# Optimization experiments

Hardware: AMD Instinct MI355X
Metric: run time of the kernel (lower is better)

## Reference

```python
import jax, jax.numpy as jnp
import numpy as np

N_NODES = 50000
IN_FT = 64
OUT_FT = 64
J = 3
MAX_SCALE = 2 ** (J - 1)  # 4
TOTAL_DIM = IN_FT * (1 + (J - 1) + J * (J - 1) // 2)  # 6*IN_FT = 384
N_EDGES = 800000


def setup_inputs() -> dict:
    key = jax.random.key(0)
    k1, k2, k3, k4, k5 = jax.random.split(key, 5)
    seq = jax.random.normal(k1, (N_NODES, IN_FT), dtype=jnp.float32)
    edge_index = jax.random.randint(k2, (2, N_EDGES), 0, N_NODES, dtype=jnp.int32)
    edge_weight = jax.random.uniform(k3, (N_EDGES,), dtype=jnp.float32)
    # xavier_normal_ with gain=1.414 on fc.weight [OUT_FT, TOTAL_DIM]
    std = 1.414 * np.sqrt(2.0 / (OUT_FT + TOTAL_DIM))
    fc_w = jax.random.normal(k4, (OUT_FT, TOTAL_DIM), dtype=jnp.float32) * std
    bias = jnp.zeros((OUT_FT,), dtype=jnp.float32)
    prelu_a = jnp.array(0.25, dtype=jnp.float32)  # nn.PReLU default single param
    return {"seq": seq, "edge_index": edge_index, "edge_weight": edge_weight,
            "fc_w": fc_w, "bias": bias, "prelu_a": prelu_a}


def reference(seq, edge_index, edge_weight, fc_w, bias, prelu_a):
    n = seq.shape[0]
    f = seq.shape[1]
    src, dst = edge_index[0], edge_index[1]

    def spmm(x):  # gather source features, scale by edge weight, scatter-add to dest
        return jax.ops.segment_sum(x[src] * edge_weight[:, None], dst, num_segments=n)

    diff_list = []
    x_curr = seq
    for step in range(1, MAX_SCALE + 1):
        x_curr = spmm(x_curr)
        if step & (step - 1) == 0:
            diff_list.append(x_curr)

    F0 = diff_list[-1]
    F1 = jnp.concatenate([jnp.abs(diff_list[i - 1] - diff_list[i])
                          for i in range(1, len(diff_list))], axis=1)

    # second-order features: diffuse concatenated U, take abs diffs of blocks
    U = jnp.concatenate(diff_list, axis=1)  # [N, J*f]
    U_diff = [U]
    for _ in range(1, MAX_SCALE):
        U_diff.append(spmm(U_diff[-1]))
    feats2 = []
    for j in range(J):
        for jp in range(j + 1, J):
            s, e = j * f, (j + 1) * f
            feats2.append(jnp.abs(U_diff[jp][:, s:e] - U_diff[jp - 1][:, s:e]))
    F2 = jnp.concatenate(feats2, axis=1)

    feats = jnp.concatenate([F0, F1, F2], axis=1)  # [N, 6*f]
    out = feats @ fc_w.T + bias
    return jnp.where(out > 0, out, prelu_a * out)
```

## Files before the change

kernel.cpp:

```cpp
#include <hip/hip_runtime.h>
#include <hip/hip_bf16.h>

typedef short short8 __attribute__((ext_vector_type(8)));
typedef float f32x4 __attribute__((ext_vector_type(4)));

static constexpr int F = 64;
static constexpr int TOT = 384;
static constexpr int SLOT = 64;
static constexpr int CAP = 1536;
static constexpr int EPB = 4096;
static constexpr int WPN = 20480;

__device__ __forceinline__ unsigned short f2bf(float f) {
    unsigned u = __builtin_bit_cast(unsigned, f);
    u += 0x7fffu + ((u >> 16) & 1u);
    return (unsigned short)(u >> 16);
}
__device__ __forceinline__ float bflo(unsigned u) {
    return __builtin_bit_cast(float, u << 16);
}
__device__ __forceinline__ float bfhi(unsigned u) {
    return __builtin_bit_cast(float, u & 0xffff0000u);
}


__global__ __launch_bounds__(256) void combo_kernel(
    const float* __restrict__ x, unsigned* __restrict__ xb,
    const float* __restrict__ fcw, unsigned short* __restrict__ wp,
    int* __restrict__ gcur, long long total8, int cvtblocks, int nbuck)
{
    int b = blockIdx.x;
    if (b < cvtblocks) {
        long long i = (long long)b * 256 + threadIdx.x;
        if (i >= total8) return;
        const float4 f0 = *(const float4*)(x + i * 8);
        const float4 f1 = *(const float4*)(x + i * 8 + 4);
        uint4 o;
        o.x = (unsigned)f2bf(f0.x) | ((unsigned)f2bf(f0.y) << 16);
        o.y = (unsigned)f2bf(f0.z) | ((unsigned)f2bf(f0.w) << 16);
        o.z = (unsigned)f2bf(f1.x) | ((unsigned)f2bf(f1.y) << 16);
        o.w = (unsigned)f2bf(f1.z) | ((unsigned)f2bf(f1.w) << 16);
        *(uint4*)(xb + i * 4) = o;
    } else if (b == cvtblocks) {
        for (int e = threadIdx.x; e < WPN; e += 256) {
            int j = e & 7;
            int l = (e >> 3) & 63;
            int t = (e >> 9) & 3;
            int s = e >> 11;
            int k  = s * 32 + ((l >> 4) << 3) + j;
            int nn = t * 16 + (l & 15);
            int c  = k & 63;
            float v;
            if (k < 64)       v = fcw[nn * TOT + c];
            else if (k < 128) v = fcw[nn * TOT + 64 + c] + fcw[nn * TOT + 192 + c];
            else if (k < 192) v = fcw[nn * TOT + 128 + c];
            else if (k < 256) v = fcw[nn * TOT + 256 + c];
            else              v = fcw[nn * TOT + 320 + c];
            wp[e] = f2bf(v);
        }
    } else {
        for (int i = threadIdx.x; i < nbuck; i += 256) gcur[i] = 0;
    }
}


__global__ __launch_bounds__(256) void scatter_bucket(
    const int* __restrict__ src, const int* __restrict__ dst,
    const float* __restrict__ ew, int* __restrict__ gcur,
    int2* __restrict__ ebuf, int ne)
{
    __shared__ int hist[1024];
    __shared__ int base[1024];
    for (int i = threadIdx.x; i < 1024; i += 256) hist[i] = 0;
    __syncthreads();

    long long b0 = (long long)blockIdx.x * EPB;
    int sv[16]; int dv[16]; float wv[16];
#pragma unroll
    for (int j = 0; j < 4; ++j) {
        long long i = b0 + (long long)(threadIdx.x + 256 * j) * 4;
        if (i + 3 < ne) {
            int4   s = *(const int4*)(src + i);
            int4   d = *(const int4*)(dst + i);
            float4 w = *(const float4*)(ew + i);
            sv[j*4+0]=s.x; sv[j*4+1]=s.y; sv[j*4+2]=s.z; sv[j*4+3]=s.w;
            dv[j*4+0]=d.x; dv[j*4+1]=d.y; dv[j*4+2]=d.z; dv[j*4+3]=d.w;
            wv[j*4+0]=w.x; wv[j*4+1]=w.y; wv[j*4+2]=w.z; wv[j*4+3]=w.w;
        } else {
#pragma unroll
            for (int c = 0; c < 4; ++c) {
                long long e = i + c;
                if (e < ne) { sv[j*4+c]=src[e]; dv[j*4+c]=dst[e]; wv[j*4+c]=ew[e]; }
                else dv[j*4+c] = -1;
            }
        }
    }
#pragma unroll
    for (int c = 0; c < 16; ++c)
        if (dv[c] >= 0) atomicAdd(&hist[dv[c] >> 6], 1);
    __syncthreads();
    for (int i = threadIdx.x; i < 1024; i += 256) {
        int h = hist[i];
        base[i] = h ? atomicAdd(&gcur[i], h) : 0;
        hist[i] = 0;
    }
    __syncthreads();
#pragma unroll
    for (int c = 0; c < 16; ++c) {
        int d = dv[c];
        if (d < 0) continue;
        int b = d >> 6;
        int p = base[b] + atomicAdd(&hist[b], 1);
        if (p < CAP)
            ebuf[(long long)b * CAP + p] =
                make_int2(sv[c] | ((d & 63) << 26), __float_as_int(wv[c]));
    }
}


__global__ __launch_bounds__(256) void bucket_to_slots(
    const int2* __restrict__ ebuf, const int* __restrict__ gcur,
    unsigned* __restrict__ csr4, int* __restrict__ cnt, int n)
{
    __shared__ int lcnt[64];
    int b = blockIdx.x;
    if (threadIdx.x < 64) lcnt[threadIdx.x] = 0;
    __syncthreads();
    int m = min(gcur[b], CAP);
    long long eb = (long long)b * CAP;
    for (int i = threadIdx.x; i < m; i += 256) {
        int2 r = ebuf[eb + i];
        int dl = (r.x >> 26) & 63;
        int s  = r.x & 0x03ffffff;
        int p  = atomicAdd(&lcnt[dl], 1);
        if (p < SLOT) {
            long long node = ((long long)b << 6) + dl;
            csr4[(node << 6) + p] =
                (unsigned)s | ((unsigned)f2bf(__int_as_float(r.y)) << 16);
        }
    }
    __syncthreads();
    if (threadIdx.x < 64) {
        int node = (b << 6) + threadIdx.x;
        if (node < n) cnt[node] = min(lcnt[threadIdx.x], SLOT);
    }
}


__global__ __launch_bounds__(256) void spmm_bf16(
    const unsigned short* __restrict__ xb, unsigned short* __restrict__ yb,
    const int* __restrict__ cnt, const unsigned* __restrict__ csr4, int n)
{
    int wid  = (blockIdx.x * 256 + threadIdx.x) >> 6;
    int lane = threadIdx.x & 63;
    if (wid >= n) return;
    int deg = min(cnt[wid], SLOT);
    long long beg = (long long)wid << 6;
    int g  = lane >> 3;
    int fi = lane & 7;

    float a0[8], a1[8];
#pragma unroll
    for (int i = 0; i < 8; ++i) { a0[i] = 0.f; a1[i] = 0.f; }

    for (int k = 0; k < deg; k += 16) {
        int e0 = k + 2 * g;
        unsigned r0 = 0u, r1 = 0u;
        if (e0 < deg) {
            uint2 rr = *(const uint2*)(csr4 + beg + e0);
            r0 = rr.x;
            if (e0 + 1 < deg) r1 = rr.y;
        }
        int   s0 = (int)(r0 & 0xffffu), s1 = (int)(r1 & 0xffffu);
        float w0 = bfhi(r0),            w1 = bfhi(r1);
        uint4 xa = *(const uint4*)(xb + (long long)s0 * F + fi * 8);
        uint4 xc = *(const uint4*)(xb + (long long)s1 * F + fi * 8);
        a0[0] += w0 * bflo(xa.x); a0[1] += w0 * bfhi(xa.x);
        a0[2] += w0 * bflo(xa.y); a0[3] += w0 * bfhi(xa.y);
        a0[4] += w0 * bflo(xa.z); a0[5] += w0 * bfhi(xa.z);
        a0[6] += w0 * bflo(xa.w); a0[7] += w0 * bfhi(xa.w);
        a1[0] += w1 * bflo(xc.x); a1[1] += w1 * bfhi(xc.x);
        a1[2] += w1 * bflo(xc.y); a1[3] += w1 * bfhi(xc.y);
        a1[4] += w1 * bflo(xc.z); a1[5] += w1 * bfhi(xc.z);
        a1[6] += w1 * bflo(xc.w); a1[7] += w1 * bfhi(xc.w);
    }
#pragma unroll
    for (int i = 0; i < 8; ++i) a0[i] += a1[i];
#pragma unroll
    for (int m = 8; m < 64; m <<= 1) {
#pragma unroll
        for (int i = 0; i < 8; ++i) a0[i] += __shfl_xor(a0[i], m, 64);
    }
    if (lane < 8) {
        uint4 o;
        o.x = (unsigned)f2bf(a0[0]) | ((unsigned)f2bf(a0[1]) << 16);
        o.y = (unsigned)f2bf(a0[2]) | ((unsigned)f2bf(a0[3]) << 16);
        o.z = (unsigned)f2bf(a0[4]) | ((unsigned)f2bf(a0[5]) << 16);
        o.w = (unsigned)f2bf(a0[6]) | ((unsigned)f2bf(a0[7]) << 16);
        *(uint4*)(yb + (long long)wid * F + fi * 8) = o;
    }
}


__global__ __launch_bounds__(256) void gemm_mfma2(
    const unsigned short* __restrict__ y1, const unsigned short* __restrict__ y2,
    const unsigned short* __restrict__ y3, const unsigned short* __restrict__ y4,
    const unsigned short* __restrict__ wp, const float* __restrict__ bias,
    const float* __restrict__ pa, float* __restrict__ out, int n)
{
    int lane = threadIdx.x & 63;
    int wid  = (blockIdx.x * 256 + threadIdx.x) >> 6;
    int m0   = wid * 16;
    if (m0 >= n) return;

    int r  = m0 + (lane & 15);
    int cb = (lane >> 4) * 8;
    float yv0[16], yv1[16], yv2[16], yv3[16];
    {
        const unsigned short* b0 = y1 + (long long)r * F;
        const unsigned short* b1 = y2 + (long long)r * F;
        const unsigned short* b2 = y3 + (long long)r * F;
        const unsigned short* b3 = y4 + (long long)r * F;
#define LOADSEG(dstv, bp)                                                     \
        {                                                                     \
            uint4 u0 = *(const uint4*)((bp) + cb);                            \
            uint4 u1 = *(const uint4*)((bp) + 32 + cb);                       \
            dstv[0]  = bflo(u0.x); dstv[1]  = bfhi(u0.x);                     \
            dstv[2]  = bflo(u0.y); dstv[3]  = bfhi(u0.y);                     \
            dstv[4]  = bflo(u0.z); dstv[5]  = bfhi(u0.z);                     \
            dstv[6]  = bflo(u0.w); dstv[7]  = bfhi(u0.w);                     \
            dstv[8]  = bflo(u1.x); dstv[9]  = bfhi(u1.x);                     \
            dstv[10] = bflo(u1.y); dstv[11] = bfhi(u1.y);                     \
            dstv[12] = bflo(u1.z); dstv[13] = bfhi(u1.z);                     \
            dstv[14] = bflo(u1.w); dstv[15] = bfhi(u1.w);                     \
        }
        LOADSEG(yv0, b0)
        LOADSEG(yv1, b1)
        LOADSEG(yv2, b2)
        LOADSEG(yv3, b3)
#undef LOADSEG
    }

    const short8* wps = (const short8*)wp;

    f32x4 acc0 = {0.f, 0.f, 0.f, 0.f};
    f32x4 acc1 = acc0, acc2 = acc0, acc3 = acc0;

#pragma unroll
    for (int s = 0; s < 10; ++s) {
        const int fb = s >> 1;
        const int h  = s & 1;
        short8 af;
#pragma unroll
        for (int j = 0; j < 8; ++j) {
            int ci = h * 8 + j;
            float fv;
            if (fb == 0)      fv = yv3[ci];
            else if (fb == 1) fv = fabsf(yv0[ci] - yv1[ci]);
            else if (fb == 2) fv = fabsf(yv1[ci] - yv3[ci]);
            else if (fb == 3) fv = fabsf(yv2[ci] - yv1[ci]);
            else              fv = fabsf(yv3[ci] - yv2[ci]);
            af[j] = (short)f2bf(fv);
        }
        short8 bf0 = wps[(s * 4 + 0) * 64 + lane];
        short8 bf1 = wps[(s * 4 + 1) * 64 + lane];
        short8 bf2 = wps[(s * 4 + 2) * 64 + lane];
        short8 bf3 = wps[(s * 4 + 3) * 64 + lane];
        acc0 = __builtin_amdgcn_mfma_f32_16x16x32_bf16(af, bf0, acc0, 0, 0, 0);
        acc1 = __builtin_amdgcn_mfma_f32_16x16x32_bf16(af, bf1, acc1, 0, 0, 0);
        acc2 = __builtin_amdgcn_mfma_f32_16x16x32_bf16(af, bf2, acc2, 0, 0, 0);
        acc3 = __builtin_amdgcn_mfma_f32_16x16x32_bf16(af, bf3, acc3, 0, 0, 0);
    }

    float a = pa[0];
    int orow = m0 + (lane >> 4) * 4;
    int ocol = lane & 15;
#define WRITE_T(accv, t)                                                      \
    {                                                                         \
        float bco = bias[(t) * 16 + ocol];                                    \
        _Pragma("unroll")                                                     \
        for (int v = 0; v < 4; ++v) {                                         \
            float val = accv[v] + bco;                                        \
            val = val > 0.f ? val : a * val;                                  \
            out[(long long)(orow + v) * F + (t) * 16 + ocol] = val;           \
        }                                                                     \
    }
    WRITE_T(acc0, 0)
    WRITE_T(acc1, 1)
    WRITE_T(acc2, 2)
    WRITE_T(acc3, 3)
#undef WRITE_T
}

extern "C" void kernel_launch(void* const* d_in, const int* in_sizes, int n_in,
                              void* d_out, int out_size, void* d_ws, size_t ws_size,
                              hipStream_t stream)
{
    const float* seq  = (const float*)d_in[0];
    const int*   eidx = (const int*)d_in[1];
    const float* ew   = (const float*)d_in[2];
    const float* fcw  = (const float*)d_in[3];
    const float* bias = (const float*)d_in[4];
    const float* pa   = (const float*)d_in[5];
    float* out = (float*)d_out;

    int n  = in_sizes[0] / F;
    int ne = in_sizes[2];
    const int* src = eidx;
    const int* dst = eidx + ne;

    long long nF = (long long)n * F;
    int nbuck = (n + 63) >> 6;

    unsigned short* xb  = (unsigned short*)d_ws;
    unsigned short* yb1 = xb  + nF;
    unsigned short* yb2 = yb1 + nF;
    unsigned short* yb3 = yb2 + nF;
    unsigned short* yb4 = yb3 + nF;
    int2* ebuf = (int2*)yb3;
    unsigned* csr4 = (unsigned*)(yb4 + nF);
    int*  cnt  = (int*)(csr4 + (long long)n * SLOT);
    int*  gcur = cnt + ((n + 3) & ~3);
    unsigned short* wp = (unsigned short*)(gcur + ((nbuck + 3) & ~3));

    long long total8 = nF / 8;
    int cvtblocks = (int)((total8 + 255) / 256);
    combo_kernel<<<cvtblocks + 2, 256, 0, stream>>>(
        seq, (unsigned*)xb, fcw, wp, gcur, total8, cvtblocks, nbuck);

    int bb = (ne + EPB - 1) / EPB;
    scatter_bucket<<<bb, 256, 0, stream>>>(src, dst, ew, gcur, ebuf, ne);
    bucket_to_slots<<<nbuck, 256, 0, stream>>>(ebuf, gcur, csr4, cnt, n);

    int sb = (int)((nF + 255) / 256);
    spmm_bf16<<<sb, 256, 0, stream>>>(xb,  yb1, cnt, csr4, n);
    spmm_bf16<<<sb, 256, 0, stream>>>(yb1, yb2, cnt, csr4, n);
    spmm_bf16<<<sb, 256, 0, stream>>>(yb2, yb3, cnt, csr4, n);
    spmm_bf16<<<sb, 256, 0, stream>>>(yb3, yb4, cnt, csr4, n);

    int gw = (n + 15) / 16;
    int gb = (gw * 64 + 255) / 256;
    gemm_mfma2<<<gb, 256, 0, stream>>>(yb1, yb2, yb3, yb4, wp, bias, pa, out, n);
}
```

Measured before the change: 140.4 us.

## Sort nodes by degree and process eight nodes per wave in SpMM

Builds a degree histogram, a prefix scan and a counting sort, so that nodes with equal degree are grouped into the same wavefront. Each wave then handles 8 nodes with 8 lanes per node, which removes the cross-lane shuffle reduction, and each lane walks its node's edges four at a time with vector loads. The goal is less divergence and less wasted lane work for the low average degree (~16). In exchange it adds two small kernels, one of them a single-threaded scan, global atomics and an indirection through the order array, and it loses the contiguous node locality of the output writes.

```diff
diff --git a/kernel.cpp b/kernel.cpp
--- a/kernel.cpp
+++ b/kernel.cpp
@@ -27,7 +27,8 @@
 __global__ __launch_bounds__(256) void combo_kernel(
     const float* __restrict__ x, unsigned* __restrict__ xb,
     const float* __restrict__ fcw, unsigned short* __restrict__ wp,
-    int* __restrict__ gcur, long long total8, int cvtblocks, int nbuck)
+    int* __restrict__ gcur, int* __restrict__ dhist, int* __restrict__ dcur,
+    long long total8, int cvtblocks, int nbuck)
 {
     int b = blockIdx.x;
     if (b < cvtblocks) {
@@ -60,6 +61,7 @@
         }
     } else {
         for (int i = threadIdx.x; i < nbuck; i += 256) gcur[i] = 0;
+        if (threadIdx.x < 65) { dhist[threadIdx.x] = 0; dcur[threadIdx.x] = 0; }
     }
 }
 
@@ -120,7 +122,8 @@
 
 __global__ __launch_bounds__(256) void bucket_to_slots(
     const int2* __restrict__ ebuf, const int* __restrict__ gcur,
-    unsigned* __restrict__ csr4, int* __restrict__ cnt, int n)
+    unsigned* __restrict__ csr4, int* __restrict__ cnt,
+    int* __restrict__ dhist, int n)
 {
     __shared__ int lcnt[64];
     int b = blockIdx.x;
@@ -142,63 +145,103 @@
     __syncthreads();
     if (threadIdx.x < 64) {
         int node = (b << 6) + threadIdx.x;
-        if (node < n) cnt[node] = min(lcnt[threadIdx.x], SLOT);
-    }
-}
-
-
-__global__ __launch_bounds__(256) void spmm_bf16(
+        if (node < n) {
+            int d = min(lcnt[threadIdx.x], SLOT);
+            cnt[node] = d;
+            atomicAdd(&dhist[d], 1);
+        }
+    }
+}
+
+
+__global__ __launch_bounds__(64) void dscan_kernel(
+    const int* __restrict__ dhist, int* __restrict__ dcur)
+{
+    if (threadIdx.x == 0) {
+        int acc = 0;
+        for (int i = 0; i < 65; ++i) { dcur[i] = acc; acc += dhist[i]; }
+    }
+}
+
+__global__ __launch_bounds__(256) void dorder_kernel(
+    const int* __restrict__ cnt, int* __restrict__ dcur,
+    int* __restrict__ order, int n)
+{
+    __shared__ int h[65], bse[65], c[65];
+    for (int i = threadIdx.x; i < 65; i += 256) h[i] = 0;
+    __syncthreads();
+    int node = blockIdx.x * 256 + threadIdx.x;
+    int d = -1;
+    if (node < n) { d = min(cnt[node], SLOT); atomicAdd(&h[d], 1); }
+    __syncthreads();
+    for (int i = threadIdx.x; i < 65; i += 256) {
+        bse[i] = h[i] ? atomicAdd(&dcur[i], h[i]) : 0;
+        c[i] = 0;
+    }
+    __syncthreads();
+    if (d >= 0) {
+        int p = bse[d] + atomicAdd(&c[d], 1);
+        order[p] = node;
+    }
+}
+
+
+__global__ __launch_bounds__(256) void spmm4(
     const unsigned short* __restrict__ xb, unsigned short* __restrict__ yb,
-    const int* __restrict__ cnt, const unsigned* __restrict__ csr4, int n)
-{
-    int wid  = (blockIdx.x * 256 + threadIdx.x) >> 6;
+    const int* __restrict__ cnt, const unsigned* __restrict__ csr4,
+    const int* __restrict__ order, int n)
+{
+    int w    = (blockIdx.x * 256 + threadIdx.x) >> 6;
     int lane = threadIdx.x & 63;
-    if (wid >= n) return;
-    int deg = min(cnt[wid], SLOT);
-    long long beg = (long long)wid << 6;
-    int g  = lane >> 3;
+    int j  = lane >> 3;
     int fi = lane & 7;
-
-    float a0[8], a1[8];
-#pragma unroll
-    for (int i = 0; i < 8; ++i) { a0[i] = 0.f; a1[i] = 0.f; }
-
-    for (int k = 0; k < deg; k += 16) {
-        int e0 = k + 2 * g;
-        unsigned r0 = 0u, r1 = 0u;
-        if (e0 < deg) {
-            uint2 rr = *(const uint2*)(csr4 + beg + e0);
-            r0 = rr.x;
-            if (e0 + 1 < deg) r1 = rr.y;
-        }
-        int   s0 = (int)(r0 & 0xffffu), s1 = (int)(r1 & 0xffffu);
-        float w0 = bfhi(r0),            w1 = bfhi(r1);
-        uint4 xa = *(const uint4*)(xb + (long long)s0 * F + fi * 8);
-        uint4 xc = *(const uint4*)(xb + (long long)s1 * F + fi * 8);
-        a0[0] += w0 * bflo(xa.x); a0[1] += w0 * bfhi(xa.x);
-        a0[2] += w0 * bflo(xa.y); a0[3] += w0 * bfhi(xa.y);
-        a0[4] += w0 * bflo(xa.z); a0[5] += w0 * bfhi(xa.z);
-        a0[6] += w0 * bflo(xa.w); a0[7] += w0 * bfhi(xa.w);
-        a1[0] += w1 * bflo(xc.x); a1[1] += w1 * bfhi(xc.x);
-        a1[2] += w1 * bflo(xc.y); a1[3] += w1 * bfhi(xc.y);
-        a1[4] += w1 * bflo(xc.z); a1[5] += w1 * bfhi(xc.z);
-        a1[6] += w1 * bflo(xc.w); a1[7] += w1 * bfhi(xc.w);
-    }
-#pragma unroll
-    for (int i = 0; i < 8; ++i) a0[i] += a1[i];
-#pragma unroll
-    for (int m = 8; m < 64; m <<= 1) {
-#pragma unroll
-        for (int i = 0; i < 8; ++i) a0[i] += __shfl_xor(a0[i], m, 64);
-    }
-    if (lane < 8) {
-        uint4 o;
-        o.x = (unsigned)f2bf(a0[0]) | ((unsigned)f2bf(a0[1]) << 16);
-        o.y = (unsigned)f2bf(a0[2]) | ((unsigned)f2bf(a0[3]) << 16);
-        o.z = (unsigned)f2bf(a0[4]) | ((unsigned)f2bf(a0[5]) << 16);
-        o.w = (unsigned)f2bf(a0[6]) | ((unsigned)f2bf(a0[7]) << 16);
-        *(uint4*)(yb + (long long)wid * F + fi * 8) = o;
-    }
+    int idx = w * 8 + j;
+    if (idx >= n) return;
+    int node = order[idx];
+    int deg  = min(cnt[node], SLOT);
+    long long base = (long long)node << 6;
+
+    float acc[8];
+#pragma unroll
+    for (int i = 0; i < 8; ++i) acc[i] = 0.f;
+
+    for (int k = 0; k < deg; k += 4) {
+        uint4 rr = *(const uint4*)(csr4 + base + k);
+        unsigned r0 = rr.x;
+        unsigned r1 = (k + 1 < deg) ? rr.y : 0u;
+        unsigned r2 = (k + 2 < deg) ? rr.z : 0u;
+        unsigned r3 = (k + 3 < deg) ? rr.w : 0u;
+        int s0 = (int)(r0 & 0xffffu), s1 = (int)(r1 & 0xffffu);
+        int s2 = (int)(r2 & 0xffffu), s3 = (int)(r3 & 0xffffu);
+        float w0 = bfhi(r0), w1 = bfhi(r1), w2 = bfhi(r2), w3 = bfhi(r3);
+        uint4 x0 = *(const uint4*)(xb + (long long)s0 * F + fi * 8);
+        uint4 x1 = *(const uint4*)(xb + (long long)s1 * F + fi * 8);
+        uint4 x2 = *(const uint4*)(xb + (long long)s2 * F + fi * 8);
+        uint4 x3 = *(const uint4*)(xb + (long long)s3 * F + fi * 8);
+        acc[0] += w0 * bflo(x0.x); acc[1] += w0 * bfhi(x0.x);
+        acc[2] += w0 * bflo(x0.y); acc[3] += w0 * bfhi(x0.y);
+        acc[4] += w0 * bflo(x0.z); acc[5] += w0 * bfhi(x0.z);
+        acc[6] += w0 * bflo(x0.w); acc[7] += w0 * bfhi(x0.w);
+        acc[0] += w1 * bflo(x1.x); acc[1] += w1 * bfhi(x1.x);
+        acc[2] += w1 * bflo(x1.y); acc[3] += w1 * bfhi(x1.y);
+        acc[4] += w1 * bflo(x1.z); acc[5] += w1 * bfhi(x1.z);
+        acc[6] += w1 * bflo(x1.w); acc[7] += w1 * bfhi(x1.w);
+        acc[0] += w2 * bflo(x2.x); acc[1] += w2 * bfhi(x2.x);
+        acc[2] += w2 * bflo(x2.y); acc[3] += w2 * bfhi(x2.y);
+        acc[4] += w2 * bflo(x2.z); acc[5] += w2 * bfhi(x2.z);
+        acc[6] += w2 * bflo(x2.w); acc[7] += w2 * bfhi(x2.w);
+        acc[0] += w3 * bflo(x3.x); acc[1] += w3 * bfhi(x3.x);
+        acc[2] += w3 * bflo(x3.y); acc[3] += w3 * bfhi(x3.y);
+        acc[4] += w3 * bflo(x3.z); acc[5] += w3 * bfhi(x3.z);
+        acc[6] += w3 * bflo(x3.w); acc[7] += w3 * bfhi(x3.w);
+    }
+
+    uint4 o;
+    o.x = (unsigned)f2bf(acc[0]) | ((unsigned)f2bf(acc[1]) << 16);
+    o.y = (unsigned)f2bf(acc[2]) | ((unsigned)f2bf(acc[3]) << 16);
+    o.z = (unsigned)f2bf(acc[4]) | ((unsigned)f2bf(acc[5]) << 16);
+    o.w = (unsigned)f2bf(acc[6]) | ((unsigned)f2bf(acc[7]) << 16);
+    *(uint4*)(yb + (long long)node * F + fi * 8) = o;
 }
 
 
@@ -322,21 +365,28 @@
     int*  cnt  = (int*)(csr4 + (long long)n * SLOT);
     int*  gcur = cnt + ((n + 3) & ~3);
     unsigned short* wp = (unsigned short*)(gcur + ((nbuck + 3) & ~3));
+    int*  dhist = (int*)(wp + WPN);
+    int*  dcur  = dhist + 68;
+    int*  order = dcur + 68;
 
     long long total8 = nF / 8;
     int cvtblocks = (int)((total8 + 255) / 256);
     combo_kernel<<<cvtblocks + 2, 256, 0, stream>>>(
-        seq, (unsigned*)xb, fcw, wp, gcur, total8, cvtblocks, nbuck);
+        seq, (unsigned*)xb, fcw, wp, gcur, dhist, dcur, total8, cvtblocks, nbuck);
 
     int bb = (ne + EPB - 1) / EPB;
     scatter_bucket<<<bb, 256, 0, stream>>>(src, dst, ew, gcur, ebuf, ne);
-    bucket_to_slots<<<nbuck, 256, 0, stream>>>(ebuf, gcur, csr4, cnt, n);
-
-    int sb = (int)((nF + 255) / 256);
-    spmm_bf16<<<sb, 256, 0, stream>>>(xb,  yb1, cnt, csr4, n);
-    spmm_bf16<<<sb, 256, 0, stream>>>(yb1, yb2, cnt, csr4, n);
-    spmm_bf16<<<sb, 256, 0, stream>>>(yb2, yb3, cnt, csr4, n);
-    spmm_bf16<<<sb, 256, 0, stream>>>(yb3, yb4, cnt, csr4, n);
+    bucket_to_slots<<<nbuck, 256, 0, stream>>>(ebuf, gcur, csr4, cnt, dhist, n);
+
+    dscan_kernel<<<1, 64, 0, stream>>>(dhist, dcur);
+    dorder_kernel<<<(n + 255) / 256, 256, 0, stream>>>(cnt, dcur, order, n);
+
+    int waves = (n + 7) / 8;
+    int sb = (waves * 64 + 255) / 256;
+    spmm4<<<sb, 256, 0, stream>>>(xb,  yb1, cnt, csr4, order, n);
+    spmm4<<<sb, 256, 0, stream>>>(yb1, yb2, cnt, csr4, order, n);
+    spmm4<<<sb, 256, 0, stream>>>(yb2, yb3, cnt, csr4, order, n);
+    spmm4<<<sb, 256, 0, stream>>>(yb3, yb4, cnt, csr4, order, n);
 
     int gw = (n + 15) / 16;
     int gb = (gw * 64 + 255) / 256;
```

New measurement: 257.4 us. +83.4%, slower.
